# Kernel optimization log

Measured on AMD Instinct MI355X. Metric: run time of the kernel, lower is better.

Reference implementation:

```python
import jax, jax.numpy as jnp
import numpy as np

D_MODEL = 1024
N_HEADS = 16
HEAD_DIM = 64
T = 4096
ROT = HEAD_DIM // 2          # 32 channels get rotary
PAIR = ROT // 2              # 16 cos/sin frequencies
EPS = 1e-6
SCALE = 0.12                 # constant attention scale (not 1/sqrt(d))
ROPE_BASE = 10000.0
VOCAB = 50257


def setup_inputs() -> dict:
    key = jax.random.key(0)
    k_x, k_qkv, k_o, k_tok = jax.random.split(key, 4)
    bound = 0.5 / np.sqrt(D_MODEL)
    x = jax.random.normal(k_x, (1, T, D_MODEL), dtype=jnp.float32)
    w_qkv = jax.random.uniform(k_qkv, (3 * D_MODEL, D_MODEL), jnp.float32, -bound, bound)
    # module uses zero_init for w_o; use small random so output is non-trivial
    w_o = jax.random.uniform(k_o, (D_MODEL, D_MODEL), jnp.float32, -bound, bound)
    q_norm_w = jnp.ones((HEAD_DIM,), jnp.float32)
    k_norm_w = jnp.ones((HEAD_DIM,), jnp.float32)
    tokens = jax.random.randint(k_tok, (1, T), 0, VOCAB, dtype=jnp.int64)
    pos = jnp.arange(T, dtype=jnp.int64)
    # RotaryCache: inv_freq over pair dims, cos/sin of t * inv_freq
    inv_freq = 1.0 / (ROPE_BASE ** (jnp.arange(PAIR, dtype=jnp.float32) / PAIR))
    freqs = jnp.arange(T, dtype=jnp.float32)[:, None] * inv_freq[None, :]  # [T, PAIR]
    return {
        "x": x, "tokens": tokens, "pos": pos,
        "w_qkv": w_qkv, "w_o": w_o,
        "q_norm_w": q_norm_w, "k_norm_w": k_norm_w,
        "cos": jnp.cos(freqs), "sin": jnp.sin(freqs),
        "window_tokens": 1024, "block_size": 128,
    }


def _rmsnorm(x, w):
    var = jnp.mean(x * x, axis=-1, keepdims=True)
    return x * jax.lax.rsqrt(var + EPS) * w


def reference(x, tokens, pos, w_qkv, w_o, q_norm_w, k_norm_w, cos, sin,
              window_tokens, block_size):
    B, Tq, C = x.shape
    H, Dh = N_HEADS, HEAD_DIM
    qkv = x @ w_qkv.T                                  # [B, T, 3C]
    q, k, v = jnp.split(qkv, 3, axis=-1)

    def to_bhtd(t):
        return t.reshape(B, Tq, H, Dh).transpose(0, 2, 1, 3)
    q, k, v = to_bhtd(q), to_bhtd(k), to_bhtd(v)

    q = _rmsnorm(q, q_norm_w)
    k = _rmsnorm(k, k_norm_w)

    # half-truncated RoPE: rotate first ROT channels pairwise (even/odd)
    c = cos[pos][None, None]                           # [1,1,T,PAIR]
    s = sin[pos][None, None]

    def rope_rotate(t):
        t1, t2 = t[..., :ROT], t[..., ROT:]
        even, odd = t1[..., 0::2], t1[..., 1::2]
        r_even = even * c - odd * s
        r_odd = even * s + odd * c
        t1r = jnp.stack([r_even, r_odd], axis=-1).reshape(t1.shape)
        return jnp.concatenate([t1r, t2], axis=-1)

    q = rope_rotate(q)
    k = rope_rotate(k)

    v = v * 0.5                                        # no value-embed branch

    scores = jnp.einsum('bhtd,bhsd->bhts', q, k) * SCALE
    idx = jnp.arange(Tq)
    diff = idx[:, None] - idx[None, :]
    allowed = (diff >= 0) & (diff < window_tokens)     # sliding causal window
    scores = jnp.where(allowed, scores, -jnp.inf)
    p = jax.nn.softmax(scores, axis=-1)
    out = jnp.einsum('bhts,bhsd->bhtd', p, v)
    out = out.transpose(0, 2, 1, 3).reshape(B, Tq, C)
    return out @ w_o.T
```

## Files before the change

### kernel.cpp

```cpp
#include <hip/hip_runtime.h>


typedef __bf16 bf16x8 __attribute__((ext_vector_type(8)));
typedef __bf16 bf16x2 __attribute__((ext_vector_type(2)));
typedef float f32x4 __attribute__((ext_vector_type(4)));
typedef unsigned short u16x8 __attribute__((ext_vector_type(8)));
typedef unsigned short u16x4 __attribute__((ext_vector_type(4)));

#define MFMA16(a, b, c) __builtin_amdgcn_mfma_f32_16x16x32_bf16((a), (b), (c), 0, 0, 0)

__device__ __forceinline__ unsigned short f2bf(float f) {
    unsigned int u = __float_as_uint(f);
    u += 0x7fffu + ((u >> 16) & 1u);
    return (unsigned short)(u >> 16);
}
__device__ __forceinline__ float bf2f(unsigned short h) {
    return __uint_as_float(((unsigned int)h) << 16);
}
__device__ __forceinline__ unsigned int pk2bf(float a, float b) {
#if __has_builtin(__builtin_amdgcn_cvt_pk_bf16_f32)
    bf16x2 v = __builtin_amdgcn_cvt_pk_bf16_f32(a, b);
    return __builtin_bit_cast(unsigned int, v);
#else
    return (unsigned int)f2bf(a) | ((unsigned int)f2bf(b) << 16);
#endif
}
__device__ __forceinline__ float fexp2(float x) {
#if __has_builtin(__builtin_amdgcn_exp2f)
    return __builtin_amdgcn_exp2f(x);
#else
    return exp2f(x);
#endif
}

__device__ __forceinline__ void gl_lds16(const void* g, void* l) {
    typedef __attribute__((address_space(1))) unsigned int GU;
    typedef __attribute__((address_space(3))) unsigned int LU;
    __builtin_amdgcn_global_load_lds((GU*)(unsigned long long)g,
                                     (LU*)(unsigned int)(unsigned long long)l,
                                     16, 0, 0);
}

__device__ __forceinline__ void wait_vm0() {
    asm volatile("s_waitcnt vmcnt(0)" ::: "memory");
}

__global__ void cvt3_kernel(const float* __restrict__ x,
                            const float* __restrict__ wqkv,
                            const float* __restrict__ wo,
                            unsigned short* __restrict__ xb,
                            unsigned short* __restrict__ wqkvb,
                            unsigned short* __restrict__ wob) {
    int i = blockIdx.x * 256 + threadIdx.x;
    const float* src;
    unsigned short* dst;
    int off;
    if (i < 1048576) { src = x; dst = xb; off = i; }
    else if (i < 1835008) { src = wqkv; dst = wqkvb; off = i - 1048576; }
    else { src = wo; dst = wob; off = i - 1835008; }
    float4 f = ((const float4*)src)[off];
    u16x4 o;
    o[0] = f2bf(f.x); o[1] = f2bf(f.y); o[2] = f2bf(f.z); o[3] = f2bf(f.w);
    ((u16x4*)dst)[off] = o;
}

#define TBS 72
__global__ __launch_bounds__(256, 3) void gemm_qkv(
    const unsigned short* __restrict__ A,
    const unsigned short* __restrict__ Bt,
    const float* __restrict__ cosb, const float* __restrict__ sinb,
    const float* __restrict__ qw, const float* __restrict__ kw,
    unsigned short* __restrict__ Qb,
    unsigned short* __restrict__ Kb,
    unsigned short* __restrict__ Vt)
{
    __shared__ unsigned short smem[16384];
    unsigned short* As0 = smem;
    unsigned short* As1 = smem + 4096;
    unsigned short* Bs0 = smem + 8192;
    unsigned short* Bs1 = smem + 12288;

    const int tid = threadIdx.x;
    const int wave = tid >> 6, lane = tid & 63;
    const int quad = lane >> 4, l16 = lane & 15;
    const int m0 = blockIdx.x * 128, n0 = blockIdx.y * 128;
    const int wm = (wave >> 1) * 64, wn = (wave & 1) * 64;

    f32x4 acc[4][4];
#pragma unroll
    for (int i = 0; i < 4; ++i)
#pragma unroll
        for (int j = 0; j < 4; ++j) acc[i][j] = (f32x4){0.f, 0.f, 0.f, 0.f};

    const int lrow = lane >> 2;
    const int lcol = ((lane & 3) ^ ((lane >> 3) & 3)) * 8;
    const int csw  = (quad ^ ((l16 >> 1) & 3)) * 8;

    for (int k0 = 0; k0 < 1024; k0 += 64) {
        {
            const unsigned short* ab = A + (size_t)(m0 + wave * 16 + lrow) * 1024 + k0 + lcol;
            gl_lds16(ab,              &As0[wave * 512]);
            gl_lds16(ab + 32,         &As1[wave * 512]);
            gl_lds16(ab + 65536,      &As0[2048 + wave * 512]);
            gl_lds16(ab + 65536 + 32, &As1[2048 + wave * 512]);
            const unsigned short* bb = Bt + (size_t)(n0 + wave * 16 + lrow) * 1024 + k0 + lcol;
            gl_lds16(bb,              &Bs0[wave * 512]);
            gl_lds16(bb + 32,         &Bs1[wave * 512]);
            gl_lds16(bb + 65536,      &Bs0[2048 + wave * 512]);
            gl_lds16(bb + 65536 + 32, &Bs1[2048 + wave * 512]);
        }
        __syncthreads();
        {
            bf16x8 af[4], bfr[4];
#pragma unroll
            for (int mt = 0; mt < 4; ++mt)
                af[mt] = *(const bf16x8*)&As0[(wm + mt * 16 + l16) * 32 + csw];
#pragma unroll
            for (int nt = 0; nt < 4; ++nt)
                bfr[nt] = *(const bf16x8*)&Bs0[(wn + nt * 16 + l16) * 32 + csw];
#pragma unroll
            for (int mt = 0; mt < 4; ++mt)
#pragma unroll
                for (int nt = 0; nt < 4; ++nt)
                    acc[mt][nt] = MFMA16(af[mt], bfr[nt], acc[mt][nt]);
        }
        {
            bf16x8 af[4], bfr[4];
#pragma unroll
            for (int mt = 0; mt < 4; ++mt)
                af[mt] = *(const bf16x8*)&As1[(wm + mt * 16 + l16) * 32 + csw];
#pragma unroll
            for (int nt = 0; nt < 4; ++nt)
                bfr[nt] = *(const bf16x8*)&Bs1[(wn + nt * 16 + l16) * 32 + csw];
#pragma unroll
            for (int mt = 0; mt < 4; ++mt)
#pragma unroll
                for (int nt = 0; nt < 4; ++nt)
                    acc[mt][nt] = MFMA16(af[mt], bfr[nt], acc[mt][nt]);
        }
        __syncthreads();
    }

    unsigned short* tbw = smem + wave * 1152;
    const int region = blockIdx.y >> 3;
    const int h = ((blockIdx.y & 7) << 1) + (wave & 1);

    if (region < 2) {
        const float* wgt = region ? kw : qw;
        unsigned short* dst = region ? Kb : Qb;
        const float post = region ? 1.f : 0.17312340490667046f;
        float w[4];
#pragma unroll
        for (int nt = 0; nt < 4; ++nt) w[nt] = wgt[nt * 16 + l16] * post;
#pragma unroll
        for (int mt = 0; mt < 4; ++mt) {
#pragma unroll
            for (int r = 0; r < 4; ++r) {
                const int row = m0 + wm + mt * 16 + quad * 4 + r;
                float ss = 0.f;
#pragma unroll
                for (int nt = 0; nt < 4; ++nt)
                    ss += acc[mt][nt][r] * acc[mt][nt][r];
                ss += __shfl_xor(ss, 1); ss += __shfl_xor(ss, 2);
                ss += __shfl_xor(ss, 4); ss += __shfl_xor(ss, 8);
                const float rn = rsqrtf(ss * (1.f / 64.f) + 1e-6f);
                float val[4];
#pragma unroll
                for (int nt = 0; nt < 4; ++nt)
                    val[nt] = acc[mt][nt][r] * rn * w[nt];
#pragma unroll
                for (int nt = 0; nt < 2; ++nt) {
                    const float prt = __shfl_xor(val[nt], 1);
                    const int p = nt * 8 + (l16 >> 1);
                    const float c = cosb[row * 16 + p];
                    const float s = sinb[row * 16 + p];
                    val[nt] = (l16 & 1) ? (prt * s + val[nt] * c)
                                        : (val[nt] * c - prt * s);
                }
#pragma unroll
                for (int nt = 0; nt < 4; ++nt)
                    tbw[(quad * 4 + r) * TBS + nt * 16 + l16] = f2bf(val[nt]);
            }
            const int t = lane >> 2, dcol = (lane & 3) * 16;
            u16x8 v0 = *(const u16x8*)&tbw[t * TBS + dcol];
            u16x8 v1 = *(const u16x8*)&tbw[t * TBS + dcol + 8];
            const size_t ob = ((size_t)h * 4096 + (m0 + wm + mt * 16 + t)) * 64 + dcol;
            *(u16x8*)&dst[ob] = v0;
            *(u16x8*)&dst[ob + 8] = v1;
        }
    } else {
#pragma unroll
        for (int mt = 0; mt < 4; ++mt) {
#pragma unroll
            for (int nt = 0; nt < 4; ++nt)
#pragma unroll
                for (int r = 0; r < 4; ++r)
                    tbw[(nt * 16 + l16) * 16 + quad * 4 + r] =
                        f2bf(acc[mt][nt][r] * 0.5f);
            u16x8 v0 = *(const u16x8*)&tbw[lane * 16];
            u16x8 v1 = *(const u16x8*)&tbw[lane * 16 + 8];
            const size_t vo = ((size_t)h * 64 + lane) * 4096 + m0 + wm + mt * 16;
            *(u16x8*)&Vt[vo] = v0;
            *(u16x8*)&Vt[vo + 8] = v1;
        }
    }
}

#define PSTR 72

template <int MASK>
__device__ __forceinline__ void qk_exp_2g(
    int sb, int qt0w, int quad, int l16, int csw, int rbase,
    const unsigned short* KsA, const unsigned short* KsB,
    unsigned short* Pw, const bf16x8 (&qf)[2][2], float (&lsum)[2])
{
#pragma unroll
    for (int i = 0; i < 4; ++i) {
        const bf16x8 kf0 = *(const bf16x8*)&KsA[(rbase + i * 16 + l16) * 32 + csw];
        const bf16x8 kf1 = *(const bf16x8*)&KsB[(rbase + i * 16 + l16) * 32 + csw];
#pragma unroll
        for (int g = 0; g < 2; ++g) {
            f32x4 z = (f32x4){0.f, 0.f, 0.f, 0.f};
            z = MFMA16(kf0, qf[g][0], z);
            z = MFMA16(kf1, qf[g][1], z);
            float p[4];
#pragma unroll
            for (int r = 0; r < 4; ++r) {
                float e = fexp2(z[r]);
                if (MASK) {
                    const int s = sb + i * 16 + quad * 4 + r;
                    e = ((unsigned)((qt0w + g * 16 + l16) - s) < 1024u) ? e : 0.f;
                }
                p[r] = e;
                lsum[g] += e;
            }
            uint2 pk;
            pk.x = pk2bf(p[0], p[1]);
            pk.y = pk2bf(p[2], p[3]);
            *(uint2*)&Pw[(g * 16 + l16) * PSTR + i * 16 + quad * 4] = pk;
        }
    }
}

__device__ __forceinline__ void pv_acc_2g(
    int quad, int l16, int csw,
    const unsigned short* VsA, const unsigned short* VsB,
    const unsigned short* Pw, f32x4 (&o)[2][4])
{
    bf16x8 pf0[2], pf1[2];
#pragma unroll
    for (int g = 0; g < 2; ++g) {
        pf0[g] = *(const bf16x8*)&Pw[(g * 16 + l16) * PSTR + quad * 8];
        pf1[g] = *(const bf16x8*)&Pw[(g * 16 + l16) * PSTR + 32 + quad * 8];
    }
    __builtin_amdgcn_s_setprio(1);
#pragma unroll
    for (int dt = 0; dt < 4; ++dt) {
        const bf16x8 vf0 = *(const bf16x8*)&VsA[(dt * 16 + l16) * 32 + csw];
        const bf16x8 vf1 = *(const bf16x8*)&VsB[(dt * 16 + l16) * 32 + csw];
#pragma unroll
        for (int g = 0; g < 2; ++g) {
            o[g][dt] = MFMA16(pf0[g], vf0, o[g][dt]);
            o[g][dt] = MFMA16(pf1[g], vf1, o[g][dt]);
        }
    }
    __builtin_amdgcn_s_setprio(0);
}

__global__ __launch_bounds__(256) void attn_kernel(
    const unsigned short* __restrict__ Qb,
    const unsigned short* __restrict__ Kb,
    const unsigned short* __restrict__ Vt,
    unsigned short* __restrict__ att)
{
    __shared__ unsigned short KsA[2][4096], KsB[2][4096];
    __shared__ unsigned short Vs0[2048], Vs1[2048];
    __shared__ unsigned short Vs2[2048], Vs3[2048];
    __shared__ unsigned short P[4][32 * PSTR];

    const int bid = blockIdx.x;
    const int h = ((bid & 7) << 1) | ((bid >> 3) & 1);
    const int t0 = (31 - (bid >> 4)) * 128;

    const int tid = threadIdx.x;
    const int wave = tid >> 6, lane = tid & 63;
    const int quad = lane >> 4, l16 = lane & 15;
    const int qt0 = t0 + wave * 32;
    const int srow = lane >> 2;
    const int scol = ((lane & 3) ^ ((lane >> 3) & 3)) * 8;
    const int csw  = (quad ^ ((l16 >> 1) & 3)) * 8;

    const unsigned short* Qh = Qb + (size_t)h * 4096 * 64;
    const unsigned short* Kh = Kb + (size_t)h * 4096 * 64;
    const unsigned short* Vh = Vt + (size_t)h * 64 * 4096;

    bf16x8 qf[2][2];
#pragma unroll
    for (int g = 0; g < 2; ++g) {
        qf[g][0] = *(const bf16x8*)&Qh[(qt0 + g * 16 + l16) * 64 + quad * 8];
        qf[g][1] = *(const bf16x8*)&Qh[(qt0 + g * 16 + l16) * 64 + 32 + quad * 8];
    }

    f32x4 o[2][4];
#pragma unroll
    for (int g = 0; g < 2; ++g)
#pragma unroll
        for (int dt = 0; dt < 4; ++dt) o[g][dt] = (f32x4){0.f, 0.f, 0.f, 0.f};
    float lsum[2] = {0.f, 0.f};
    unsigned short* Pw = P[wave];

    auto stageK = [&](int b, int s) {
        if (wave < 2) {
#pragma unroll
            for (int l = 0; l < 4; ++l) {
                const int rg = wave * 4 + l;
                const unsigned short* kb =
                    Kh + (size_t)(s + rg * 16 + srow) * 64 + scol;
                gl_lds16(kb,      &KsA[b][rg * 512]);
                gl_lds16(kb + 32, &KsB[b][rg * 512]);
            }
        }
    };
    auto stageV = [&](int s) {
        if (wave >= 2) {
            const int w2 = wave - 2;
#pragma unroll
            for (int l = 0; l < 2; ++l) {
                const int dg = w2 * 2 + l;
                const unsigned short* vb =
                    Vh + (size_t)(dg * 16 + srow) * 4096 + s + scol;
                gl_lds16(vb,      &Vs0[dg * 512]);
                gl_lds16(vb + 32, &Vs1[dg * 512]);
                gl_lds16(vb + 64, &Vs2[dg * 512]);
                gl_lds16(vb + 96, &Vs3[dg * 512]);
            }
        }
    };

    const int s_lo = (t0 >= 1024) ? (t0 - 1024) : 0;
    const int NT = ((t0 - s_lo) >> 7) + 1;

    stageK(0, s_lo);
    if (wave < 2) wait_vm0();
    __builtin_amdgcn_s_barrier();
    __builtin_amdgcn_sched_barrier(0);
    int buf = 0;
    for (int n = 0; n < NT; ++n) {
        const int s0 = s_lo + n * 128;
        const int sb1 = s0 + 64;
        if (n + 1 < NT) stageK(buf ^ 1, s0 + 128);
        stageV(s0);
        const bool d0 = (s0 + 63 < qt0 - 1023);
        const bool c0 = (s0 + 63 <= qt0) && (s0 >= qt0 - 992);
        const bool d1 = (sb1 > qt0 + 31) || (sb1 + 63 < qt0 - 1023);
        const bool c1 = (sb1 + 63 <= qt0) && (sb1 >= qt0 - 992);
        if (!d0) {
            if (c0) qk_exp_2g<0>(s0, qt0, quad, l16, csw, 0, KsA[buf], KsB[buf],
                                 Pw, qf, lsum);
            else    qk_exp_2g<1>(s0, qt0, quad, l16, csw, 0, KsA[buf], KsB[buf],
                                 Pw, qf, lsum);
        }
        if (wave >= 2) wait_vm0();
        __builtin_amdgcn_s_barrier();
        __builtin_amdgcn_sched_barrier(0);
        if (!d0) pv_acc_2g(quad, l16, csw, Vs0, Vs1, Pw, o);
        if (!d1) {
            if (c1) qk_exp_2g<0>(sb1, qt0, quad, l16, csw, 64, KsA[buf], KsB[buf],
                                 Pw, qf, lsum);
            else    qk_exp_2g<1>(sb1, qt0, quad, l16, csw, 64, KsA[buf], KsB[buf],
                                 Pw, qf, lsum);
            pv_acc_2g(quad, l16, csw, Vs2, Vs3, Pw, o);
        }
        if (wave < 2) wait_vm0();
        __builtin_amdgcn_s_barrier();
        __builtin_amdgcn_sched_barrier(0);
        buf ^= 1;
    }

#pragma unroll
    for (int g = 0; g < 2; ++g) {
        float ls = lsum[g];
        ls += __shfl_xor(ls, 16);
        ls += __shfl_xor(ls, 32);
        float lr[4];
#pragma unroll
        for (int r = 0; r < 4; ++r) lr[r] = 1.f / __shfl(ls, quad * 4 + r);
#pragma unroll
        for (int dt = 0; dt < 4; ++dt)
#pragma unroll
            for (int r = 0; r < 4; ++r)
                att[(size_t)(qt0 + g * 16 + quad * 4 + r) * 1024 +
                    h * 64 + dt * 16 + l16] = f2bf(o[g][dt][r] * lr[r]);
    }
}

__global__ __launch_bounds__(256) void gemm_out(
    const unsigned short* __restrict__ A,
    const unsigned short* __restrict__ Bt,
    float* __restrict__ C)
{
    __shared__ unsigned short As0[2][2048], As1[2][2048];
    __shared__ unsigned short Bs0[2][4096], Bs1[2][4096];
    const int tid = threadIdx.x;
    const int wave = tid >> 6, lane = tid & 63;
    const int quad = lane >> 4, l16 = lane & 15;
    const int m0 = blockIdx.x * 64, n0 = blockIdx.y * 128;
    const int wm = (wave >> 1) * 32, wn = (wave & 1) * 64;
    const int lrow = lane >> 2;
    const int lcol = ((lane & 3) ^ ((lane >> 3) & 3)) * 8;
    const int csw  = (quad ^ ((l16 >> 1) & 3)) * 8;

    f32x4 acc[2][4];
#pragma unroll
    for (int i = 0; i < 2; ++i)
#pragma unroll
        for (int j = 0; j < 4; ++j) acc[i][j] = (f32x4){0.f, 0.f, 0.f, 0.f};

    auto stage = [&](int buf, int k0) {
        const unsigned short* ab = A + (size_t)(m0 + wave * 16 + lrow) * 1024 + k0 + lcol;
        gl_lds16(ab,      &As0[buf][wave * 512]);
        gl_lds16(ab + 32, &As1[buf][wave * 512]);
#pragma unroll
        for (int i = 0; i < 2; ++i) {
            const int c = wave * 2 + i;
            const unsigned short* bb = Bt + (size_t)(n0 + c * 16 + lrow) * 1024 + k0 + lcol;
            gl_lds16(bb,      &Bs0[buf][c * 512]);
            gl_lds16(bb + 32, &Bs1[buf][c * 512]);
        }
    };

    stage(0, 0);
    __syncthreads();
    int buf = 0;
    for (int k0 = 0; k0 < 1024; k0 += 64) {
        if (k0 + 64 < 1024) stage(buf ^ 1, k0 + 64);
        {
            bf16x8 af[2], bfr[4];
#pragma unroll
            for (int mt = 0; mt < 2; ++mt)
                af[mt] = *(const bf16x8*)&As0[buf][(wm + mt * 16 + l16) * 32 + csw];
#pragma unroll
            for (int nt = 0; nt < 4; ++nt)
                bfr[nt] = *(const bf16x8*)&Bs0[buf][(wn + nt * 16 + l16) * 32 + csw];
#pragma unroll
            for (int mt = 0; mt < 2; ++mt)
#pragma unroll
                for (int nt = 0; nt < 4; ++nt)
                    acc[mt][nt] = MFMA16(af[mt], bfr[nt], acc[mt][nt]);
        }
        {
            bf16x8 af[2], bfr[4];
#pragma unroll
            for (int mt = 0; mt < 2; ++mt)
                af[mt] = *(const bf16x8*)&As1[buf][(wm + mt * 16 + l16) * 32 + csw];
#pragma unroll
            for (int nt = 0; nt < 4; ++nt)
                bfr[nt] = *(const bf16x8*)&Bs1[buf][(wn + nt * 16 + l16) * 32 + csw];
#pragma unroll
            for (int mt = 0; mt < 2; ++mt)
#pragma unroll
                for (int nt = 0; nt < 4; ++nt)
                    acc[mt][nt] = MFMA16(af[mt], bfr[nt], acc[mt][nt]);
        }
        __syncthreads();
        buf ^= 1;
    }
#pragma unroll
    for (int mt = 0; mt < 2; ++mt)
#pragma unroll
        for (int nt = 0; nt < 4; ++nt)
#pragma unroll
            for (int r = 0; r < 4; ++r) {
                const int row = m0 + wm + mt * 16 + quad * 4 + r;
                const int col = n0 + wn + nt * 16 + l16;
                C[(size_t)row * 1024 + col] = acc[mt][nt][r];
            }
}

extern "C" void kernel_launch(void* const* d_in, const int* in_sizes, int n_in,
                              void* d_out, int out_size, void* d_ws, size_t ws_size,
                              hipStream_t stream) {
    const float* x    = (const float*)d_in[0];
    const float* wqkv = (const float*)d_in[3];
    const float* wo   = (const float*)d_in[4];
    const float* qw   = (const float*)d_in[5];
    const float* kw   = (const float*)d_in[6];
    const float* cosb = (const float*)d_in[7];
    const float* sinb = (const float*)d_in[8];

    char* ws = (char*)d_ws;
    if (ws_size < (size_t)48 * 1024 * 1024) return;
    unsigned short* xb    = (unsigned short*)(ws + ((size_t)0 << 20));
    unsigned short* wqkvb = (unsigned short*)(ws + ((size_t)8 << 20));
    unsigned short* wob   = (unsigned short*)(ws + ((size_t)14 << 20));
    unsigned short* Qb    = (unsigned short*)(ws + ((size_t)16 << 20));
    unsigned short* Kb    = (unsigned short*)(ws + ((size_t)24 << 20));
    unsigned short* Vt    = (unsigned short*)(ws + ((size_t)32 << 20));
    unsigned short* attb  = (unsigned short*)(ws + ((size_t)40 << 20));

    cvt3_kernel<<<8192, 256, 0, stream>>>(x, wqkv, wo, xb, wqkvb, wob);

    gemm_qkv<<<dim3(32, 24), 256, 0, stream>>>(xb, wqkvb, cosb, sinb, qw, kw,
                                               Qb, Kb, Vt);

    attn_kernel<<<512, 256, 0, stream>>>(Qb, Kb, Vt, attb);

    gemm_out<<<dim3(64, 8), 256, 0, stream>>>(attb, wob, (float*)d_out);
}
```

Measured before the change: 173.3 us.

## Compute softmax row sums via MFMA with ones and permute V/P layouts

Replaces the scalar per-element accumulation of softmax denominators (and the final cross-lane shuffle reduction) with an extra MFMA of P against a ones vector, so the row sums land in the output layout directly. P tiles are now written as 16-byte stores combining two 16-column chunks, and the V-transpose store in the projection kernel is permuted to match. These permutations must keep the K-dimension ordering of P and V consistent for PV. The aim is fewer VALU adds and wider LDS stores, in exchange for extra MFMA work and bf16-rounded P being used in the denominator.

```diff
diff --git a/kernel.cpp b/kernel.cpp
--- a/kernel.cpp
+++ b/kernel.cpp
@@ -31,6 +31,12 @@
 #else
     return exp2f(x);
 #endif
+}
+__device__ __forceinline__ bf16x8 ones_bf16x8() {
+    u16x8 u;
+#pragma unroll
+    for (int j = 0; j < 8; ++j) u[j] = 0x3F80;
+    return __builtin_bit_cast(bf16x8, u);
 }
 
 __device__ __forceinline__ void gl_lds16(const void* g, void* l) {
@@ -197,11 +203,12 @@
                 for (int r = 0; r < 4; ++r)
                     tbw[(nt * 16 + l16) * 16 + quad * 4 + r] =
                         f2bf(acc[mt][nt][r] * 0.5f);
-            u16x8 v0 = *(const u16x8*)&tbw[lane * 16];
-            u16x8 v1 = *(const u16x8*)&tbw[lane * 16 + 8];
-            const size_t vo = ((size_t)h * 64 + lane) * 4096 + m0 + wm + mt * 16;
-            *(u16x8*)&Vt[vo] = v0;
-            *(u16x8*)&Vt[vo + 8] = v1;
+            const size_t vo = ((size_t)h * 64 + lane) * 4096 + m0 + wm;
+#pragma unroll
+            for (int q = 0; q < 4; ++q) {
+                u16x4 vq = *(const u16x4*)&tbw[lane * 16 + q * 4];
+                *(u16x4*)&Vt[vo + q * 16 + mt * 4] = vq;
+            }
         }
     }
 }
@@ -212,8 +219,9 @@
 __device__ __forceinline__ void qk_exp_2g(
     int sb, int qt0w, int quad, int l16, int csw, int rbase,
     const unsigned short* KsA, const unsigned short* KsB,
-    unsigned short* Pw, const bf16x8 (&qf)[2][2], float (&lsum)[2])
+    unsigned short* Pw, const bf16x8 (&qf)[2][2])
 {
+    uint2 hold[2];
 #pragma unroll
     for (int i = 0; i < 4; ++i) {
         const bf16x8 kf0 = *(const bf16x8*)&KsA[(rbase + i * 16 + l16) * 32 + csw];
@@ -232,12 +240,17 @@
                     e = ((unsigned)((qt0w + g * 16 + l16) - s) < 1024u) ? e : 0.f;
                 }
                 p[r] = e;
-                lsum[g] += e;
             }
             uint2 pk;
             pk.x = pk2bf(p[0], p[1]);
             pk.y = pk2bf(p[2], p[3]);
-            *(uint2*)&Pw[(g * 16 + l16) * PSTR + i * 16 + quad * 4] = pk;
+            if (i == 0 || i == 2) {
+                hold[g] = pk;
+            } else {
+                uint4 w4;
+                w4.x = hold[g].x; w4.y = hold[g].y; w4.z = pk.x; w4.w = pk.y;
+                *(uint4*)&Pw[(g * 16 + l16) * PSTR + quad * 16 + (i == 3 ? 8 : 0)] = w4;
+            }
         }
     }
 }
@@ -245,7 +258,7 @@
 __device__ __forceinline__ void pv_acc_2g(
     int quad, int l16, int csw,
     const unsigned short* VsA, const unsigned short* VsB,
-    const unsigned short* Pw, f32x4 (&o)[2][4])
+    const unsigned short* Pw, f32x4 (&o)[2][4], f32x4 (&ls)[2])
 {
     bf16x8 pf0[2], pf1[2];
 #pragma unroll
@@ -253,7 +266,13 @@
         pf0[g] = *(const bf16x8*)&Pw[(g * 16 + l16) * PSTR + quad * 8];
         pf1[g] = *(const bf16x8*)&Pw[(g * 16 + l16) * PSTR + 32 + quad * 8];
     }
+    const bf16x8 ones = ones_bf16x8();
     __builtin_amdgcn_s_setprio(1);
+#pragma unroll
+    for (int g = 0; g < 2; ++g) {
+        ls[g] = MFMA16(pf0[g], ones, ls[g]);
+        ls[g] = MFMA16(pf1[g], ones, ls[g]);
+    }
 #pragma unroll
     for (int dt = 0; dt < 4; ++dt) {
         const bf16x8 vf0 = *(const bf16x8*)&VsA[(dt * 16 + l16) * 32 + csw];
@@ -302,11 +321,13 @@
     }
 
     f32x4 o[2][4];
-#pragma unroll
-    for (int g = 0; g < 2; ++g)
+    f32x4 ls[2];
+#pragma unroll
+    for (int g = 0; g < 2; ++g) {
+        ls[g] = (f32x4){0.f, 0.f, 0.f, 0.f};
 #pragma unroll
         for (int dt = 0; dt < 4; ++dt) o[g][dt] = (f32x4){0.f, 0.f, 0.f, 0.f};
-    float lsum[2] = {0.f, 0.f};
+    }
     unsigned short* Pw = P[wave];
 
     auto stageK = [&](int b, int s) {
@@ -356,20 +377,20 @@
         const bool c1 = (sb1 + 63 <= qt0) && (sb1 >= qt0 - 992);
         if (!d0) {
             if (c0) qk_exp_2g<0>(s0, qt0, quad, l16, csw, 0, KsA[buf], KsB[buf],
-                                 Pw, qf, lsum);
+                                 Pw, qf);
             else    qk_exp_2g<1>(s0, qt0, quad, l16, csw, 0, KsA[buf], KsB[buf],
-                                 Pw, qf, lsum);
+                                 Pw, qf);
         }
         if (wave >= 2) wait_vm0();
         __builtin_amdgcn_s_barrier();
         __builtin_amdgcn_sched_barrier(0);
-        if (!d0) pv_acc_2g(quad, l16, csw, Vs0, Vs1, Pw, o);
+        if (!d0) pv_acc_2g(quad, l16, csw, Vs0, Vs1, Pw, o, ls);
         if (!d1) {
             if (c1) qk_exp_2g<0>(sb1, qt0, quad, l16, csw, 64, KsA[buf], KsB[buf],
-                                 Pw, qf, lsum);
+                                 Pw, qf);
             else    qk_exp_2g<1>(sb1, qt0, quad, l16, csw, 64, KsA[buf], KsB[buf],
-                                 Pw, qf, lsum);
-            pv_acc_2g(quad, l16, csw, Vs2, Vs3, Pw, o);
+                                 Pw, qf);
+            pv_acc_2g(quad, l16, csw, Vs2, Vs3, Pw, o, ls);
         }
         if (wave < 2) wait_vm0();
         __builtin_amdgcn_s_barrier();
@@ -379,12 +400,9 @@
 
 #pragma unroll
     for (int g = 0; g < 2; ++g) {
-        float ls = lsum[g];
-        ls += __shfl_xor(ls, 16);
-        ls += __shfl_xor(ls, 32);
         float lr[4];
 #pragma unroll
-        for (int r = 0; r < 4; ++r) lr[r] = 1.f / __shfl(ls, quad * 4 + r);
+        for (int r = 0; r < 4; ++r) lr[r] = 1.f / ls[g][r];
 #pragma unroll
         for (int dt = 0; dt < 4; ++dt)
 #pragma unroll
```

New measurement: 173.3 us, median of 2. No clear change (+0.0%).
